# Kernel optimization log

Measured on AMD Instinct MI355X. Metric: run time of the kernel, lower is better.

The kernel has to match this reference:

```python
import math
import jax, jax.numpy as jnp
import numpy as np


def get_alibi_slopes(n_heads: int) -> jnp.ndarray:
    def _pow2_slopes(n):
        i = jnp.arange(1, n + 1, dtype=jnp.float32)
        return jnp.power(2.0, -8.0 * i / n)
    if n_heads & (n_heads - 1) == 0:
        return _pow2_slopes(n_heads)
    nearest = 2 ** math.ceil(math.log2(n_heads))
    full = _pow2_slopes(nearest)
    half = nearest // 2
    half_slopes = _pow2_slopes(half)
    extra = full[jnp.arange(half) * 2 + 1]
    return jnp.concatenate([half_slopes, extra])[:n_heads]


def build_alibi_bias(n_heads: int, T: int, causal: bool = True) -> jnp.ndarray:
    slopes = get_alibi_slopes(n_heads)  # (H,)
    idx = jnp.arange(T)
    rel = jnp.abs(idx[:, None] - idx[None, :]).astype(jnp.float32)  # (T,T)
    bias = -slopes[:, None, None] * rel[None]  # (H,T,T)
    if causal:
        future = idx[None, :] > idx[:, None]
        bias = jnp.where(future[None], -jnp.inf, bias)
    return bias


def setup_inputs() -> dict:
    key = jax.random.key(0)
    ks = jax.random.split(key, 5)
    B, T, C = 2, 2048, 1024
    s = 0.02
    return {
        "x": jax.random.normal(ks[0], (B, T, C), dtype=jnp.float32),
        "Wq": jax.random.normal(ks[1], (C, C), dtype=jnp.float32) * s,
        "Wk": jax.random.normal(ks[2], (C, C), dtype=jnp.float32) * s,
        "Wv": jax.random.normal(ks[3], (C, C), dtype=jnp.float32) * s,
        "Wo": jax.random.normal(ks[4], (C, C), dtype=jnp.float32) * s,
    }


def reference(x, Wq, Wk, Wv, Wo):
    B, T, C = x.shape
    H = 16
    D = C // H
    scale = D ** -0.5
    # torch nn.Linear(bias=False): y = x @ W.T
    def proj_split(W):
        t = jnp.einsum('btc,dc->btd', x, W)
        return t.reshape(B, T, H, D).transpose(0, 2, 1, 3)  # (B,H,T,D)
    q, k, v = proj_split(Wq), proj_split(Wk), proj_split(Wv)
    scores = jnp.einsum('bhtd,bhsd->bhts', q, k) * scale  # (B,H,T,T)
    bias = build_alibi_bias(H, T, causal=True)  # (H,T,T)
    scores = scores + bias[None]
    attn = jax.nn.softmax(scores, axis=-1)
    out = jnp.einsum('bhts,bhsd->bhtd', attn, v)
    out = out.transpose(0, 2, 1, 3).reshape(B, T, C)
    return jnp.einsum('btc,dc->btd', out, Wo)
```

## Files before the change

### kernel.cpp

```cpp
#include <hip/hip_runtime.h>
#include <hip/hip_bf16.h>


typedef _Float16 f16;
typedef f16 f16x2 __attribute__((ext_vector_type(2)));
typedef f16 f16x4 __attribute__((ext_vector_type(4)));
typedef f16 f16x8 __attribute__((ext_vector_type(8)));
typedef float f32x4 __attribute__((ext_vector_type(4)));

#define LOG2E 1.4426950408889634f
#define LDK 40
#define LDA 72
#define LDV 132

__device__ __forceinline__ f16x4 pk4(f32x4 v) {
  f16x2 a = __builtin_bit_cast(f16x2, __builtin_amdgcn_cvt_pkrtz(v[0], v[1]));
  f16x2 b = __builtin_bit_cast(f16x2, __builtin_amdgcn_cvt_pkrtz(v[2], v[3]));
  f16x4 r; r[0] = a[0]; r[1] = a[1]; r[2] = b[0]; r[3] = b[1];
  return r;
}

template <int AM>
__device__ __forceinline__ void gemm_core(const void* __restrict__ Av,
                                          const float* __restrict__ W,
                                          int m0, int n0,
                                          f16* lA, f16* lW,
                                          f32x4 acc[4][4]) {
  const int tid = threadIdx.x;
  const int lane = tid & 63, w = tid >> 6;
  const int wm = w & 1, wn = w >> 1;
  const int q = lane & 15, quad = lane >> 4;
  const int r32 = tid >> 3, k32 = (tid & 7) * 4;
  const int r16 = tid >> 2, k16 = (tid & 3) * 8;

  f32x4 wR[4], aR4[4];
  f16x8 aR8[2];
#pragma unroll
  for (int it = 0; it < 4; it++)
    wR[it] = *(const f32x4*)(W + (n0 + it * 32 + r32) * 1024 + k32);
  if (AM == 2) {
#pragma unroll
    for (int it = 0; it < 4; it++)
      aR4[it] = *(const f32x4*)((const float*)Av + (m0 + it * 32 + r32) * 1024 + k32);
  } else {
#pragma unroll
    for (int it = 0; it < 2; it++)
      aR8[it] = *(const f16x8*)((const f16*)Av + (m0 + it * 64 + r16) * 1024 + k16);
  }

  for (int kt = 0; kt < 1024; kt += 32) {
    __syncthreads();
#pragma unroll
    for (int it = 0; it < 4; it++)
      *(f16x4*)(lW + (it * 32 + r32) * LDK + k32) = pk4(wR[it]);
    if (AM == 2) {
#pragma unroll
      for (int it = 0; it < 4; it++)
        *(f16x4*)(lA + (it * 32 + r32) * LDK + k32) = pk4(aR4[it]);
    } else {
#pragma unroll
      for (int it = 0; it < 2; it++)
        *(f16x8*)(lA + (it * 64 + r16) * LDK + k16) = aR8[it];
    }
    __syncthreads();
    if (kt + 32 < 1024) {
      const int kn = kt + 32;
#pragma unroll
      for (int it = 0; it < 4; it++)
        wR[it] = *(const f32x4*)(W + (n0 + it * 32 + r32) * 1024 + kn + k32);
      if (AM == 2) {
#pragma unroll
        for (int it = 0; it < 4; it++)
          aR4[it] = *(const f32x4*)((const float*)Av + (m0 + it * 32 + r32) * 1024 + kn + k32);
      } else {
#pragma unroll
        for (int it = 0; it < 2; it++)
          aR8[it] = *(const f16x8*)((const f16*)Av + (m0 + it * 64 + r16) * 1024 + kn + k16);
      }
    }
    f16x8 aF[4], bF[4];
#pragma unroll
    for (int mt = 0; mt < 4; mt++)
      aF[mt] = *(const f16x8*)(lA + (wm * 64 + mt * 16 + q) * LDK + quad * 8);
#pragma unroll
    for (int nt = 0; nt < 4; nt++)
      bF[nt] = *(const f16x8*)(lW + (wn * 64 + nt * 16 + q) * LDK + quad * 8);
#pragma unroll
    for (int mt = 0; mt < 4; mt++)
#pragma unroll
      for (int nt = 0; nt < 4; nt++)
        acc[mt][nt] = __builtin_amdgcn_mfma_f32_16x16x32_f16(aF[mt], bF[nt], acc[mt][nt], 0, 0, 0);
  }
}

__global__ __launch_bounds__(256) void qkv_proj(
    const float* __restrict__ x, const float* __restrict__ wq,
    const float* __restrict__ wk, const float* __restrict__ wv,
    f16* __restrict__ qb, f16* __restrict__ kb, f16* __restrict__ vb,
    float qscale) {
  __shared__ __align__(16) f16 lA[128 * LDK];
  __shared__ __align__(16) f16 lW[128 * LDK];
  const int m0 = blockIdx.x * 128, n0 = blockIdx.y * 128;
  const int z = blockIdx.z;
  const float* W = (z == 0) ? wq : (z == 1) ? wk : wv;
  f16* out = (z == 0) ? qb : (z == 1) ? kb : vb;
  const float scale = (z == 0) ? qscale : 1.0f;

  f32x4 acc[4][4];
  const f32x4 zero = {0.f, 0.f, 0.f, 0.f};
#pragma unroll
  for (int i = 0; i < 4; i++)
#pragma unroll
    for (int j = 0; j < 4; j++) acc[i][j] = zero;
  gemm_core<2>(x, W, m0, n0, lA, lW, acc);

  const int tid = threadIdx.x, lane = tid & 63, w = tid >> 6;
  const int wm = w & 1, wn = w >> 1, q = lane & 15, quad = lane >> 4;
#pragma unroll
  for (int mt = 0; mt < 4; mt++)
#pragma unroll
    for (int nt = 0; nt < 4; nt++) {
      int n = n0 + wn * 64 + nt * 16 + q;
      int h = n >> 6, d = n & 63;
#pragma unroll
      for (int r = 0; r < 4; r++) {
        int mm = m0 + wm * 64 + mt * 16 + quad * 4 + r;
        int bb = mm >> 11, tl = mm & 2047;
        out[((bb * 16 + h) * 2048 + tl) * 64 + d] = (f16)(acc[mt][nt][r] * scale);
      }
    }
}

__global__ __launch_bounds__(256) void attn(
    const f16* __restrict__ qB, const f16* __restrict__ kB,
    const f16* __restrict__ vB, f16* __restrict__ att) {
  __shared__ __align__(16) f16 lK[128 * LDA];
  __shared__ __align__(16) f16 lV[64 * LDV];
  const int tid = threadIdx.x, lane = tid & 63, w = tid >> 6;
  const int q = lane & 15, quad = lane >> 4;
  const int qb_ = 31 - blockIdx.x, bh = blockIdx.y;
  const int b = bh >> 4, h = bh & 15;
  const int q0 = qb_ * 64;
  const int kv_end = q0 + 64;
  const f16* qP = qB + (bh * 2048) * 64;
  const f16* kP = kB + (bh * 2048) * 64;
  const f16* vP = vB + (bh * 2048) * 64;

  const float slope2 = __builtin_amdgcn_exp2f(-0.5f * (float)(h + 1)) * LOG2E;
  const int qg = q0 + w * 16 + q;

  f16x8 qF[2];
#pragma unroll
  for (int ks = 0; ks < 2; ks++)
    qF[ks] = *(const f16x8*)(qP + qg * 64 + ks * 32 + quad * 8);

  const f32x4 cinit = {-8.f, -8.f, -8.f, -8.f};
  f32x4 ot[4];
#pragma unroll
  for (int i = 0; i < 4; i++) ot[i] = {0.f, 0.f, 0.f, 0.f};
  float lsum = 0.0f;

  const int kr = tid >> 3, ks8 = (tid & 7) * 8;
  const int vp = (tid & 31) * 4, vd = (tid >> 5) * 8;

  f16x8 kreg[4], vreg[4];
#pragma unroll
  for (int it = 0; it < 4; it++)
    kreg[it] = *(const f16x8*)(kP + (it * 32 + kr) * 64 + ks8);
#pragma unroll
  for (int r4 = 0; r4 < 4; r4++)
    vreg[r4] = *(const f16x8*)(vP + (vp + r4) * 64 + vd);

  const int nstage = (kv_end + 127) >> 7;
  for (int st = 0; st < nstage; st++) {
    const int kv0 = st << 7;
    __syncthreads();
#pragma unroll
    for (int it = 0; it < 4; it++)
      *(f16x8*)(lK + (it * 32 + kr) * LDA + ks8) = kreg[it];
#pragma unroll
    for (int j = 0; j < 8; j++) {
      f16x4 t;
      t[0] = vreg[0][j]; t[1] = vreg[1][j]; t[2] = vreg[2][j]; t[3] = vreg[3][j];
      *(f16x4*)(lV + (vd + j) * LDV + vp) = t;
    }
    __syncthreads();
    if (st + 1 < nstage) {
      const int kn = kv0 + 128;
#pragma unroll
      for (int it = 0; it < 4; it++)
        kreg[it] = *(const f16x8*)(kP + (kn + it * 32 + kr) * 64 + ks8);
#pragma unroll
      for (int r4 = 0; r4 < 4; r4++)
        vreg[r4] = *(const f16x8*)(vP + (kn + vp + r4) * 64 + vd);
    }
#pragma unroll
    for (int half = 0; half < 2; half++) {
      const int kvh = kv0 + half * 64;
      if (kvh >= kv_end) break;
      f32x4 stv[4];
#pragma unroll
      for (int sub = 0; sub < 4; sub++) {
        const f16* kb_ = lK + (half * 64 + sub * 16 + q) * LDA + quad * 8;
        f16x8 k0 = *(const f16x8*)(kb_);
        f16x8 k1 = *(const f16x8*)(kb_ + 32);
        f32x4 a = __builtin_amdgcn_mfma_f32_16x16x32_f16(k0, qF[0], cinit, 0, 0, 0);
        a = __builtin_amdgcn_mfma_f32_16x16x32_f16(k1, qF[1], a, 0, 0, 0);
        stv[sub] = a;
      }
      const int dQ = qg - kvh;
      const bool needmask = (kvh == q0);
      f16x4 pF[4];
#pragma unroll
      for (int sub = 0; sub < 4; sub++) {
        f32x4 ev;
#pragma unroll
        for (int r = 0; r < 4; r++) {
          float dd = (float)(dQ - (sub * 16 + quad * 4 + r));
          float val = fmaf(-slope2, dd, stv[sub][r]);
          if (needmask) val = (dd >= 0.0f) ? val : -3e38f;
          ev[r] = __builtin_amdgcn_exp2f(val);
        }
        lsum += (ev[0] + ev[1]) + (ev[2] + ev[3]);
        pF[sub] = pk4(ev);
      }
#pragma unroll
      for (int sub = 0; sub < 4; sub++)
#pragma unroll
        for (int dt = 0; dt < 4; dt++) {
          f16x4 vF = *(const f16x4*)(lV + (dt * 16 + q) * LDV + half * 64 + sub * 16 + quad * 4);
          ot[dt] = __builtin_amdgcn_mfma_f32_16x16x16f16(vF, pF[sub], ot[dt], 0, 0, 0);
        }
    }
  }

  lsum += __shfl_xor(lsum, 16);
  lsum += __shfl_xor(lsum, 32);
  const float inv = 1.0f / lsum;

  __syncthreads();
  f16* OT = lK + w * (16 * LDA);
#pragma unroll
  for (int dt = 0; dt < 4; dt++) {
    f16x4 o4;
#pragma unroll
    for (int r = 0; r < 4; r++) o4[r] = (f16)(ot[dt][r] * inv);
    *(f16x4*)(OT + q * LDA + dt * 16 + quad * 4) = o4;
  }
  __syncthreads();
  const int row = lane >> 2, cs = lane & 3;
  f16x8 o8a = *(const f16x8*)(OT + row * LDA + cs * 16);
  f16x8 o8b = *(const f16x8*)(OT + row * LDA + cs * 16 + 8);
  f16* dst = att + (b * 2048 + q0 + w * 16 + row) * 1024 + h * 64 + cs * 16;
  *(f16x8*)dst = o8a;
  *(f16x8*)(dst + 8) = o8b;
}

__global__ __launch_bounds__(256) void out_proj(
    const f16* __restrict__ att, const float* __restrict__ wo,
    float* __restrict__ out) {
  __shared__ __align__(16) f16 lA[128 * LDK];
  __shared__ __align__(16) f16 lW[128 * LDK];
  const int m0 = blockIdx.x * 128, n0 = blockIdx.y * 128;
  f32x4 acc[4][4];
  const f32x4 zero = {0.f, 0.f, 0.f, 0.f};
#pragma unroll
  for (int i = 0; i < 4; i++)
#pragma unroll
    for (int j = 0; j < 4; j++) acc[i][j] = zero;
  gemm_core<0>(att, wo, m0, n0, lA, lW, acc);

  const int tid = threadIdx.x, lane = tid & 63, w = tid >> 6;
  const int wm = w & 1, wn = w >> 1, q = lane & 15, quad = lane >> 4;
#pragma unroll
  for (int mt = 0; mt < 4; mt++)
#pragma unroll
    for (int nt = 0; nt < 4; nt++) {
      int n = n0 + wn * 64 + nt * 16 + q;
#pragma unroll
      for (int r = 0; r < 4; r++) {
        int mm = m0 + wm * 64 + mt * 16 + quad * 4 + r;
        out[mm * 1024 + n] = acc[mt][nt][r];
      }
    }
}

extern "C" void kernel_launch(void* const* d_in, const int* in_sizes, int n_in,
                              void* d_out, int out_size, void* d_ws, size_t ws_size,
                              hipStream_t stream) {
  const float* x  = (const float*)d_in[0];
  const float* Wq = (const float*)d_in[1];
  const float* Wk = (const float*)d_in[2];
  const float* Wv = (const float*)d_in[3];
  const float* Wo = (const float*)d_in[4];
  char* ws = (char*)d_ws;
  const size_t MB = 1024 * 1024;
  f16* qb  = (f16*)(ws);
  f16* kb  = (f16*)(ws + 8 * MB);
  f16* vb  = (f16*)(ws + 16 * MB);
  f16* att = (f16*)(ws + 24 * MB);

  qkv_proj<<<dim3(32, 8, 3), 256, 0, stream>>>(x, Wq, Wk, Wv, qb, kb, vb,
                                               0.125f * LOG2E);
  attn<<<dim3(32, 32), 256, 0, stream>>>(qb, kb, vb, att);
  out_proj<<<dim3(32, 8), 256, 0, stream>>>(att, Wo, (float*)d_out);
}
```

Measured before the change: 221.5 us.

## Pre-convert inputs to fp16, use direct global-to-LDS loads, widen attention blocks

A new kernel converts x and all weights to fp16 up front. The GEMM core then stages tiles with global_load_lds straight into unpadded shared memory, dropping the register prefetch and in-loop fp32-to-fp16 conversion. The attention kernel now uses 512-thread blocks covering 128 query rows, so each staged K/V tile is shared by twice as many waves. The cost is an extra conversion pass and workspace traffic, plus the loss of register double-buffering and padding in the GEMM, which may add LDS bank conflicts and load stalls.

```diff
diff --git a/kernel.cpp b/kernel.cpp
--- a/kernel.cpp
+++ b/kernel.cpp
@@ -9,9 +9,14 @@
 typedef float f32x4 __attribute__((ext_vector_type(4)));
 
 #define LOG2E 1.4426950408889634f
-#define LDK 40
 #define LDA 72
 #define LDV 132
+
+typedef const __attribute__((address_space(1))) unsigned int* gas1;
+typedef __attribute__((address_space(3))) unsigned int* las3;
+__device__ __forceinline__ void gload16(const f16* g, f16* l) {
+  __builtin_amdgcn_global_load_lds((gas1)g, (las3)l, 16, 0, 0);
+}
 
 __device__ __forceinline__ f16x4 pk4(f32x4 v) {
   f16x2 a = __builtin_bit_cast(f16x2, __builtin_amdgcn_cvt_pkrtz(v[0], v[1]));
@@ -20,9 +25,33 @@
   return r;
 }
 
-template <int AM>
-__device__ __forceinline__ void gemm_core(const void* __restrict__ Av,
-                                          const float* __restrict__ W,
+__global__ __launch_bounds__(256) void cvt_f32_f16(
+    const float* __restrict__ x, const float* __restrict__ wq,
+    const float* __restrict__ wk, const float* __restrict__ wv,
+    const float* __restrict__ wo,
+    f16* __restrict__ dx, f16* __restrict__ dwq, f16* __restrict__ dwk,
+    f16* __restrict__ dwv, f16* __restrict__ dwo) {
+  const float* src; f16* dst; int n;
+  switch (blockIdx.y) {
+    case 0:  src = x;  dst = dx;  n = 4194304; break;
+    case 1:  src = wq; dst = dwq; n = 1048576; break;
+    case 2:  src = wk; dst = dwk; n = 1048576; break;
+    case 3:  src = wv; dst = dwv; n = 1048576; break;
+    default: src = wo; dst = dwo; n = 1048576; break;
+  }
+  int i = (blockIdx.x * 256 + (int)threadIdx.x) * 8;
+  if (i >= n) return;
+  f32x4 a = *(const f32x4*)(src + i);
+  f32x4 b = *(const f32x4*)(src + i + 4);
+  f16x8 o;
+  f16x4 lo4 = pk4(a), hi4 = pk4(b);
+#pragma unroll
+  for (int j = 0; j < 4; j++) { o[j] = lo4[j]; o[j + 4] = hi4[j]; }
+  *(f16x8*)(dst + i) = o;
+}
+
+__device__ __forceinline__ void gemm_core(const f16* __restrict__ A,
+                                          const f16* __restrict__ W,
                                           int m0, int n0,
                                           f16* lA, f16* lW,
                                           f32x4 acc[4][4]) {
@@ -30,61 +59,25 @@
   const int lane = tid & 63, w = tid >> 6;
   const int wm = w & 1, wn = w >> 1;
   const int q = lane & 15, quad = lane >> 4;
-  const int r32 = tid >> 3, k32 = (tid & 7) * 4;
-  const int r16 = tid >> 2, k16 = (tid & 3) * 8;
-
-  f32x4 wR[4], aR4[4];
-  f16x8 aR8[2];
-#pragma unroll
-  for (int it = 0; it < 4; it++)
-    wR[it] = *(const f32x4*)(W + (n0 + it * 32 + r32) * 1024 + k32);
-  if (AM == 2) {
-#pragma unroll
-    for (int it = 0; it < 4; it++)
-      aR4[it] = *(const f32x4*)((const float*)Av + (m0 + it * 32 + r32) * 1024 + k32);
-  } else {
-#pragma unroll
-    for (int it = 0; it < 2; it++)
-      aR8[it] = *(const f16x8*)((const f16*)Av + (m0 + it * 64 + r16) * 1024 + k16);
-  }
+  const int lrow = lane >> 2, lcol = (lane & 3) * 8;
 
   for (int kt = 0; kt < 1024; kt += 32) {
     __syncthreads();
 #pragma unroll
-    for (int it = 0; it < 4; it++)
-      *(f16x4*)(lW + (it * 32 + r32) * LDK + k32) = pk4(wR[it]);
-    if (AM == 2) {
-#pragma unroll
-      for (int it = 0; it < 4; it++)
-        *(f16x4*)(lA + (it * 32 + r32) * LDK + k32) = pk4(aR4[it]);
-    } else {
-#pragma unroll
-      for (int it = 0; it < 2; it++)
-        *(f16x8*)(lA + (it * 64 + r16) * LDK + k16) = aR8[it];
+    for (int t = 0; t < 2; t++) {
+      const int slot = t * 4 + w;
+      const int row = slot * 16 + lrow;
+      gload16(A + (m0 + row) * 1024 + kt + lcol, lA + slot * 512);
+      gload16(W + (n0 + row) * 1024 + kt + lcol, lW + slot * 512);
     }
     __syncthreads();
-    if (kt + 32 < 1024) {
-      const int kn = kt + 32;
-#pragma unroll
-      for (int it = 0; it < 4; it++)
-        wR[it] = *(const f32x4*)(W + (n0 + it * 32 + r32) * 1024 + kn + k32);
-      if (AM == 2) {
-#pragma unroll
-        for (int it = 0; it < 4; it++)
-          aR4[it] = *(const f32x4*)((const float*)Av + (m0 + it * 32 + r32) * 1024 + kn + k32);
-      } else {
-#pragma unroll
-        for (int it = 0; it < 2; it++)
-          aR8[it] = *(const f16x8*)((const f16*)Av + (m0 + it * 64 + r16) * 1024 + kn + k16);
-      }
-    }
     f16x8 aF[4], bF[4];
 #pragma unroll
     for (int mt = 0; mt < 4; mt++)
-      aF[mt] = *(const f16x8*)(lA + (wm * 64 + mt * 16 + q) * LDK + quad * 8);
+      aF[mt] = *(const f16x8*)(lA + (wm * 64 + mt * 16 + q) * 32 + quad * 8);
 #pragma unroll
     for (int nt = 0; nt < 4; nt++)
-      bF[nt] = *(const f16x8*)(lW + (wn * 64 + nt * 16 + q) * LDK + quad * 8);
+      bF[nt] = *(const f16x8*)(lW + (wn * 64 + nt * 16 + q) * 32 + quad * 8);
 #pragma unroll
     for (int mt = 0; mt < 4; mt++)
 #pragma unroll
@@ -94,15 +87,15 @@
 }
 
 __global__ __launch_bounds__(256) void qkv_proj(
-    const float* __restrict__ x, const float* __restrict__ wq,
-    const float* __restrict__ wk, const float* __restrict__ wv,
+    const f16* __restrict__ x16, const f16* __restrict__ wq16,
+    const f16* __restrict__ wk16, const f16* __restrict__ wv16,
     f16* __restrict__ qb, f16* __restrict__ kb, f16* __restrict__ vb,
     float qscale) {
-  __shared__ __align__(16) f16 lA[128 * LDK];
-  __shared__ __align__(16) f16 lW[128 * LDK];
+  __shared__ __align__(16) f16 lA[128 * 32];
+  __shared__ __align__(16) f16 lW[128 * 32];
   const int m0 = blockIdx.x * 128, n0 = blockIdx.y * 128;
   const int z = blockIdx.z;
-  const float* W = (z == 0) ? wq : (z == 1) ? wk : wv;
+  const f16* W = (z == 0) ? wq16 : (z == 1) ? wk16 : wv16;
   f16* out = (z == 0) ? qb : (z == 1) ? kb : vb;
   const float scale = (z == 0) ? qscale : 1.0f;
 
@@ -112,7 +105,7 @@
   for (int i = 0; i < 4; i++)
 #pragma unroll
     for (int j = 0; j < 4; j++) acc[i][j] = zero;
-  gemm_core<2>(x, W, m0, n0, lA, lW, acc);
+  gemm_core(x16, W, m0, n0, lA, lW, acc);
 
   const int tid = threadIdx.x, lane = tid & 63, w = tid >> 6;
   const int wm = w & 1, wn = w >> 1, q = lane & 15, quad = lane >> 4;
@@ -131,23 +124,23 @@
     }
 }
 
-__global__ __launch_bounds__(256) void attn(
+__global__ __launch_bounds__(512) void attn(
     const f16* __restrict__ qB, const f16* __restrict__ kB,
     const f16* __restrict__ vB, f16* __restrict__ att) {
   __shared__ __align__(16) f16 lK[128 * LDA];
   __shared__ __align__(16) f16 lV[64 * LDV];
   const int tid = threadIdx.x, lane = tid & 63, w = tid >> 6;
   const int q = lane & 15, quad = lane >> 4;
-  const int qb_ = 31 - blockIdx.x, bh = blockIdx.y;
+  const int qb_ = 15 - (int)blockIdx.x, bh = blockIdx.y;
   const int b = bh >> 4, h = bh & 15;
-  const int q0 = qb_ * 64;
-  const int kv_end = q0 + 64;
+  const int q0 = qb_ * 128;
   const f16* qP = qB + (bh * 2048) * 64;
   const f16* kP = kB + (bh * 2048) * 64;
   const f16* vP = vB + (bh * 2048) * 64;
 
   const float slope2 = __builtin_amdgcn_exp2f(-0.5f * (float)(h + 1)) * LOG2E;
   const int qg = q0 + w * 16 + q;
+  const int diag_kvh = q0 + (w >> 2) * 64;
 
   f16x8 qF[2];
 #pragma unroll
@@ -161,43 +154,42 @@
   float lsum = 0.0f;
 
   const int kr = tid >> 3, ks8 = (tid & 7) * 8;
-  const int vp = (tid & 31) * 4, vd = (tid >> 5) * 8;
-
-  f16x8 kreg[4], vreg[4];
-#pragma unroll
-  for (int it = 0; it < 4; it++)
-    kreg[it] = *(const f16x8*)(kP + (it * 32 + kr) * 64 + ks8);
-#pragma unroll
-  for (int r4 = 0; r4 < 4; r4++)
-    vreg[r4] = *(const f16x8*)(vP + (vp + r4) * 64 + vd);
-
-  const int nstage = (kv_end + 127) >> 7;
+  const int vp = (tid & 63) * 2, vd = (tid >> 6) * 8;
+
+  f16x8 kreg[2], vreg[2];
+#pragma unroll
+  for (int it = 0; it < 2; it++)
+    kreg[it] = *(const f16x8*)(kP + (it * 64 + kr) * 64 + ks8);
+#pragma unroll
+  for (int r2 = 0; r2 < 2; r2++)
+    vreg[r2] = *(const f16x8*)(vP + (vp + r2) * 64 + vd);
+
+  const int nstage = qb_ + 1;
   for (int st = 0; st < nstage; st++) {
     const int kv0 = st << 7;
     __syncthreads();
 #pragma unroll
-    for (int it = 0; it < 4; it++)
-      *(f16x8*)(lK + (it * 32 + kr) * LDA + ks8) = kreg[it];
+    for (int it = 0; it < 2; it++)
+      *(f16x8*)(lK + (it * 64 + kr) * LDA + ks8) = kreg[it];
 #pragma unroll
     for (int j = 0; j < 8; j++) {
-      f16x4 t;
-      t[0] = vreg[0][j]; t[1] = vreg[1][j]; t[2] = vreg[2][j]; t[3] = vreg[3][j];
-      *(f16x4*)(lV + (vd + j) * LDV + vp) = t;
+      f16x2 t; t[0] = vreg[0][j]; t[1] = vreg[1][j];
+      *(f16x2*)(lV + (vd + j) * LDV + vp) = t;
     }
     __syncthreads();
     if (st + 1 < nstage) {
       const int kn = kv0 + 128;
 #pragma unroll
-      for (int it = 0; it < 4; it++)
-        kreg[it] = *(const f16x8*)(kP + (kn + it * 32 + kr) * 64 + ks8);
-#pragma unroll
-      for (int r4 = 0; r4 < 4; r4++)
-        vreg[r4] = *(const f16x8*)(vP + (kn + vp + r4) * 64 + vd);
+      for (int it = 0; it < 2; it++)
+        kreg[it] = *(const f16x8*)(kP + (kn + it * 64 + kr) * 64 + ks8);
+#pragma unroll
+      for (int r2 = 0; r2 < 2; r2++)
+        vreg[r2] = *(const f16x8*)(vP + (kn + vp + r2) * 64 + vd);
     }
 #pragma unroll
     for (int half = 0; half < 2; half++) {
       const int kvh = kv0 + half * 64;
-      if (kvh >= kv_end) break;
+      if (kvh > diag_kvh) break;
       f32x4 stv[4];
 #pragma unroll
       for (int sub = 0; sub < 4; sub++) {
@@ -209,7 +201,7 @@
         stv[sub] = a;
       }
       const int dQ = qg - kvh;
-      const bool needmask = (kvh == q0);
+      const bool needmask = (kvh == diag_kvh);
       f16x4 pF[4];
 #pragma unroll
       for (int sub = 0; sub < 4; sub++) {
@@ -257,10 +249,10 @@
 }
 
 __global__ __launch_bounds__(256) void out_proj(
-    const f16* __restrict__ att, const float* __restrict__ wo,
+    const f16* __restrict__ att, const f16* __restrict__ wo16,
     float* __restrict__ out) {
-  __shared__ __align__(16) f16 lA[128 * LDK];
-  __shared__ __align__(16) f16 lW[128 * LDK];
+  __shared__ __align__(16) f16 lA[128 * 32];
+  __shared__ __align__(16) f16 lW[128 * 32];
   const int m0 = blockIdx.x * 128, n0 = blockIdx.y * 128;
   f32x4 acc[4][4];
   const f32x4 zero = {0.f, 0.f, 0.f, 0.f};
@@ -268,7 +260,7 @@
   for (int i = 0; i < 4; i++)
 #pragma unroll
     for (int j = 0; j < 4; j++) acc[i][j] = zero;
-  gemm_core<0>(att, wo, m0, n0, lA, lW, acc);
+  gemm_core(att, wo16, m0, n0, lA, lW, acc);
 
   const int tid = threadIdx.x, lane = tid & 63, w = tid >> 6;
   const int wm = w & 1, wn = w >> 1, q = lane & 15, quad = lane >> 4;
@@ -295,13 +287,20 @@
   const float* Wo = (const float*)d_in[4];
   char* ws = (char*)d_ws;
   const size_t MB = 1024 * 1024;
-  f16* qb  = (f16*)(ws);
-  f16* kb  = (f16*)(ws + 8 * MB);
-  f16* vb  = (f16*)(ws + 16 * MB);
-  f16* att = (f16*)(ws + 24 * MB);
-
-  qkv_proj<<<dim3(32, 8, 3), 256, 0, stream>>>(x, Wq, Wk, Wv, qb, kb, vb,
-                                               0.125f * LOG2E);
-  attn<<<dim3(32, 32), 256, 0, stream>>>(qb, kb, vb, att);
-  out_proj<<<dim3(32, 8), 256, 0, stream>>>(att, Wo, (float*)d_out);
-}
+  f16* x16  = (f16*)(ws);
+  f16* qb   = (f16*)(ws + 8 * MB);
+  f16* kb   = (f16*)(ws + 16 * MB);
+  f16* vb   = (f16*)(ws + 24 * MB);
+  f16* wq16 = (f16*)(ws + 32 * MB);
+  f16* wk16 = (f16*)(ws + 34 * MB);
+  f16* wv16 = (f16*)(ws + 36 * MB);
+  f16* wo16 = (f16*)(ws + 38 * MB);
+  f16* att  = x16;
+
+  cvt_f32_f16<<<dim3(2048, 5), 256, 0, stream>>>(x, Wq, Wk, Wv, Wo,
+                                                 x16, wq16, wk16, wv16, wo16);
+  qkv_proj<<<dim3(32, 8, 3), 256, 0, stream>>>(x16, wq16, wk16, wv16,
+                                               qb, kb, vb, 0.125f * LOG2E);
+  attn<<<dim3(16, 32), 512, 0, stream>>>(qb, kb, vb, att);
+  out_proj<<<dim3(32, 8), 256, 0, stream>>>(att, wo16, (float*)d_out);
+}
```

Measured after the change: 202.6 us. -8.5%, faster.
